# Performance work log

Hardware: AMD Instinct MI355X
Metric: run time of the kernel (lower is better)

Reference implementation:

```python
import jax, jax.numpy as jnp
import numpy as np

B, C, NS, NP = 8, 128, 32, 128  # batch, channels, nsample, npoint


def setup_inputs() -> dict:
    key = jax.random.key(0)
    k1, k2 = jax.random.split(key)
    points = jax.random.normal(k1, (B, C, NS, NP), dtype=jnp.float32)
    gamma = jax.random.uniform(k2, (1,), dtype=jnp.float32)
    return {"points": points, "gamma": gamma}


def reference(points, gamma):
    b, c, ns, npnt = points.shape
    x = points.reshape(b, c, ns * npnt)              # [B, C, N]
    # energy[b, n, m] = sum_c x[b,c,n] * x[b,c,m]   (QK^T with Q=K=x^T)
    energy = jnp.einsum('bcn,bcm->bnm', x, x)
    # max-subtraction variant: softmax(max_row - energy)
    energy_new = jnp.max(energy, axis=-1, keepdims=True) - energy
    attention = jax.nn.softmax(energy_new, axis=-1)   # [B, N, N]
    # points_attention = V @ attention^T : out[b,c,n] = sum_m x[b,c,m]*attn[b,n,m]
    out = jnp.einsum('bcm,bnm->bcn', x, attention)
    out = out.reshape(b, c, ns, npnt)
    return gamma * out + points
```

## Files before the change

kernel.cpp:

```cpp
#include <hip/hip_runtime.h>
#include <stdint.h>

#define NB_ 8
#define NC_ 128
#define NN_ 4096

typedef float f32x4 __attribute__((ext_vector_type(4)));
typedef _Float16 f16x8 __attribute__((ext_vector_type(8)));
typedef short s16x8 __attribute__((ext_vector_type(8)));
typedef unsigned short u16x4 __attribute__((ext_vector_type(4)));

__device__ __forceinline__ uint16_t f2bf(float f) {
    union { float f; uint32_t u; } v; v.f = f;
    return (uint16_t)((v.u + 0x7FFFu + ((v.u >> 16) & 1u)) >> 16);
}
__device__ __forceinline__ uint16_t f2bf_trunc(float f) {
    union { float f; uint32_t u; } v; v.f = f;
    return (uint16_t)(v.u >> 16);
}
__device__ __forceinline__ float bf2f(uint16_t b) {
    union { uint32_t u; float f; } v; v.u = ((uint32_t)b) << 16;
    return v.f;
}

__global__ __launch_bounds__(256) void prep_kernel(
        const float* __restrict__ pts, _Float16* __restrict__ xt,
        _Float16* __restrict__ Kf, uint16_t* __restrict__ Vf) {
    __shared__ float T[64][65];
    int bid = blockIdx.x;
    int ct = bid & 1, nt = (bid >> 1) & 63, b = bid >> 7;
    int c0 = ct * 64, n0 = nt * 64;
    int lr = threadIdx.x >> 6, lc = threadIdx.x & 63;
    const float* src = pts + ((size_t)b * NC_ + c0) * NN_ + n0;
#pragma unroll
    for (int r = 0; r < 16; ++r) {
        int cl = r * 4 + lr;
        T[cl][lc] = src[(size_t)cl * NN_ + lc];
    }
    __syncthreads();
#pragma unroll
    for (int r = 0; r < 16; ++r) {
        int nl = r * 4 + lr;
        xt[((size_t)b * NN_ + n0 + nl) * NC_ + c0 + lc] = (_Float16)T[lc][nl];
    }

    int w = threadIdx.x >> 6, l = threadIdx.x & 63, l15 = l & 15, g = l >> 4;
    _Float16* Kfb = Kf + (size_t)b * 524288;
    uint16_t* Vfb = Vf + (size_t)b * 524288;
#pragma unroll
    for (int e = 0; e < 2; ++e) {
        int q2 = w + e * 4;
        int tl = q2 >> 2, msq = (q2 >> 1) & 1, ccl = q2 & 1;
        int t = nt * 2 + tl, cc = ct * 2 + ccl;
        f16x8 kv;
#pragma unroll
        for (int j = 0; j < 8; ++j)
            kv[j] = (_Float16)T[ccl * 32 + g * 8 + j][tl * 32 + msq * 16 + l15];
        *(f16x8*)(Kfb + (((size_t)t * 8 + msq * 4 + cc) * 64 + l) * 8) = kv;
    }
#pragma unroll
    for (int e = 0; e < 2; ++e) {
        int q2 = w + e * 4;
        int tl = q2 >> 2, csl = q2 & 3;
        int t = nt * 2 + tl, cs = ct * 4 + csl;
        s16x8 vv;
#pragma unroll
        for (int j = 0; j < 8; ++j) {
            int m = (j < 4) ? (g * 4 + j) : (16 + g * 4 + (j - 4));
            vv[j] = (short)f2bf(T[csl * 16 + l15][tl * 32 + m]);
        }
        *(s16x8*)(Vfb + (((size_t)t * 8 + cs) * 64 + l) * 8) = vv;
    }
}

template <int MSPLIT>
__global__ __launch_bounds__(256, 3) void flash_kernel(
        const _Float16* __restrict__ xt, const _Float16* __restrict__ Kf,
        const uint16_t* __restrict__ Vf,
        uint16_t* __restrict__ Opart, float* __restrict__ lpart,
        const float* __restrict__ pts, const float* __restrict__ gamma,
        float* __restrict__ out) {
    int bid = blockIdx.x;
    int b = bid & 7;
    int rest = bid >> 3;
    int nb = rest & 31;
    int mh = rest >> 5;
    int tid = threadIdx.x;
    int w = tid >> 6, l = tid & 63, l15 = l & 15, g = l >> 4;

    __shared__ __align__(16) uint16_t Kt[2 * 4096];
    __shared__ __align__(16) uint16_t Vt[2 * 4096];

    int nbase = nb * 128 + w * 32;
    const _Float16* xtb = xt + (size_t)b * NN_ * NC_;
    const char* KfB = (const char*)(Kf + (size_t)b * 524288);
    const char* VfB = (const char*)(Vf + (size_t)b * 524288);
    char* KtB = (char*)Kt;
    char* VtB = (char*)Vt;
    int so = tid * 16;

#define STAGE(TILE, BUF) do {                                                          \
        size_t gb_ = (size_t)(TILE) * 8192 + so;                                       \
        int lb_ = (BUF) * 8192 + so;                                                   \
        __builtin_amdgcn_global_load_lds(                                              \
            (const __attribute__((address_space(1))) void*)(KfB + gb_),                \
            (__attribute__((address_space(3))) void*)(KtB + lb_), 16, 0, 0);           \
        __builtin_amdgcn_global_load_lds(                                              \
            (const __attribute__((address_space(1))) void*)(KfB + gb_ + 4096),         \
            (__attribute__((address_space(3))) void*)(KtB + lb_ + 4096), 16, 0, 0);    \
        __builtin_amdgcn_global_load_lds(                                              \
            (const __attribute__((address_space(1))) void*)(VfB + gb_),                \
            (__attribute__((address_space(3))) void*)(VtB + lb_), 16, 0, 0);           \
        __builtin_amdgcn_global_load_lds(                                              \
            (const __attribute__((address_space(1))) void*)(VfB + gb_ + 4096),         \
            (__attribute__((address_space(3))) void*)(VtB + lb_ + 4096), 16, 0, 0);    \
    } while (0)

    f16x8 q[2][4];
#pragma unroll
    for (int ns = 0; ns < 2; ++ns)
#pragma unroll
        for (int cc = 0; cc < 4; ++cc)
            q[ns][cc] = *(const f16x8*)(xtb + (size_t)(nbase + ns * 16 + l15) * NC_ + cc * 32 + g * 8);

    f32x4 acc[8][2];
#pragma unroll
    for (int cs = 0; cs < 8; ++cs)
#pragma unroll
        for (int ns = 0; ns < 2; ++ns)
            acc[cs][ns] = (f32x4){0.f, 0.f, 0.f, 0.f};
    float lsum[2] = {0.f, 0.f};

    const int nsteps = (MSPLIT == 3) ? (mh < 2 ? 43 : 42) : 128;
    const int tile0 = (MSPLIT == 3) ? (mh * 43) : 0;

    STAGE(tile0, 0);

    for (int it = 0; it < nsteps; ++it) {
        __syncthreads();
        int cur = it & 1, nxt = cur ^ 1;
        if (it + 1 < nsteps) STAGE(tile0 + it + 1, nxt);

        const _Float16* Kc = (const _Float16*)(Kt + cur * 4096);
        const uint16_t* Vc = Vt + cur * 4096;

        s16x8 pf[2];
#pragma unroll
        for (int ms = 0; ms < 2; ++ms) {
            f16x8 kf[4];
#pragma unroll
            for (int cc = 0; cc < 4; ++cc)
                kf[cc] = *(const f16x8*)(Kc + (ms * 4 + cc) * 512 + l * 8);

            f32x4 s[2];
            s[0] = (f32x4){0.f, 0.f, 0.f, 0.f};
            s[1] = (f32x4){0.f, 0.f, 0.f, 0.f};
            __builtin_amdgcn_s_setprio(1);
#pragma unroll
            for (int cc = 0; cc < 4; ++cc)
#pragma unroll
                for (int ns = 0; ns < 2; ++ns)
                    s[ns] = __builtin_amdgcn_mfma_f32_16x16x32_f16(kf[cc], q[ns][cc], s[ns], 0, 0, 0);
            __builtin_amdgcn_s_setprio(0);
#pragma unroll
            for (int ns = 0; ns < 2; ++ns) {
                float p0 = __expf(-(s[ns][0] + 64.f));
                float p1 = __expf(-(s[ns][1] + 64.f));
                float p2 = __expf(-(s[ns][2] + 64.f));
                float p3 = __expf(-(s[ns][3] + 64.f));
                lsum[ns] += (p0 + p1) + (p2 + p3);
                pf[ns][ms * 4 + 0] = (short)f2bf_trunc(p0);
                pf[ns][ms * 4 + 1] = (short)f2bf_trunc(p1);
                pf[ns][ms * 4 + 2] = (short)f2bf_trunc(p2);
                pf[ns][ms * 4 + 3] = (short)f2bf_trunc(p3);
            }
        }

        __builtin_amdgcn_s_setprio(1);
#pragma unroll
        for (int cs = 0; cs < 8; ++cs) {
            s16x8 vf = *(const s16x8*)(Vc + cs * 512 + l * 8);
#pragma unroll
            for (int ns = 0; ns < 2; ++ns)
                acc[cs][ns] = __builtin_amdgcn_mfma_f32_16x16x32_bf16(vf, pf[ns], acc[cs][ns], 0, 0, 0);
        }
        __builtin_amdgcn_s_setprio(0);
    }
#undef STAGE

    float lred[2], linv[2];
#pragma unroll
    for (int ns = 0; ns < 2; ++ns) {
        float v2 = lsum[ns];
        v2 += __shfl_xor(v2, 16);
        v2 += __shfl_xor(v2, 32);
        lred[ns] = v2;
        linv[ns] = 1.0f / v2;
    }

    if (MSPLIT > 1) {
        uint16_t* opb = Opart + (size_t)((b * 32 + nb) * MSPLIT + mh) * 16384;
#pragma unroll
        for (int cs = 0; cs < 8; ++cs)
#pragma unroll
            for (int ns = 0; ns < 2; ++ns)
#pragma unroll
                for (int r = 0; r < 4; ++r)
                    opb[(cs * 16 + g * 4 + r) * 128 + w * 32 + ns * 16 + l15] =
                        f2bf(acc[cs][ns][r] * linv[ns]);
        if (g == 0) {
            size_t lb = (size_t)((b * 32 + nb) * MSPLIT + mh) * 128;
#pragma unroll
            for (int ns = 0; ns < 2; ++ns)
                lpart[lb + w * 32 + ns * 16 + l15] = lred[ns];
        }
    } else {
        float gm = gamma[0];
        const float* ptsb = pts + (size_t)b * NC_ * NN_;
        float* outb = out + (size_t)b * NC_ * NN_;
#pragma unroll
        for (int cs = 0; cs < 8; ++cs)
#pragma unroll
            for (int ns = 0; ns < 2; ++ns)
#pragma unroll
                for (int r = 0; r < 4; ++r) {
                    size_t idx = (size_t)(cs * 16 + g * 4 + r) * NN_ + nbase + ns * 16 + l15;
                    outb[idx] = gm * acc[cs][ns][r] * linv[ns] + ptsb[idx];
                }
    }
}

template <int NS>
__global__ __launch_bounds__(256) void epi_kernel(
        const float* __restrict__ pts, const float* __restrict__ gamma,
        const uint16_t* __restrict__ Opart, const float* __restrict__ lpart,
        float* __restrict__ out) {
    size_t t = (size_t)blockIdx.x * 256 + threadIdx.x;
    size_t e = t * 4;
    int b = (int)(e >> 19);
    int r = (int)(e & 524287);
    int c = r >> 12;
    int n = r & 4095;
    int nb = n >> 7, nl = n & 127;
    int base = (b * 32 + nb) * NS;
    f32x4 osum = (f32x4){0.f, 0.f, 0.f, 0.f};
    f32x4 lsum = (f32x4){0.f, 0.f, 0.f, 0.f};
#pragma unroll
    for (int i = 0; i < NS; ++i) {
        u16x4 o16 = *(const u16x4*)(Opart + (size_t)(base + i) * 16384 + c * 128 + nl);
        f32x4 li = *(const f32x4*)(lpart + (size_t)(base + i) * 128 + nl);
#pragma unroll
        for (int j = 0; j < 4; ++j) {
            osum[j] += bf2f(o16[j]) * li[j];
            lsum[j] += li[j];
        }
    }
    f32x4 p = *(const f32x4*)(pts + e);
    float gm = gamma[0];
    f32x4 res;
#pragma unroll
    for (int j = 0; j < 4; ++j)
        res[j] = gm * osum[j] / lsum[j] + p[j];
    *(f32x4*)(out + e) = res;
}

extern "C" void kernel_launch(void* const* d_in, const int* in_sizes, int n_in,
                              void* d_out, int out_size, void* d_ws, size_t ws_size,
                              hipStream_t stream) {
    const float* pts = (const float*)d_in[0];
    const float* gamma = (const float*)d_in[1];
    float* out = (float*)d_out;

    char* ws = (char*)d_ws;
    _Float16* xt = (_Float16*)ws;
    _Float16* Kf = (_Float16*)(ws + 8388608);
    uint16_t* Vf = (uint16_t*)(ws + 16777216);
    uint16_t* Opart = (uint16_t*)(ws + 25165824);
    float* lpart = (float*)(ws + 25165824 + 25165824);
    const size_t WS3 = 25165824ull + 25165824ull + 393216ull;

    prep_kernel<<<1024, 256, 0, stream>>>(pts, xt, Kf, Vf);
    if (ws_size >= WS3) {
        flash_kernel<3><<<768, 256, 0, stream>>>(xt, Kf, Vf, Opart, lpart, pts, gamma, out);
        epi_kernel<3><<<4096, 256, 0, stream>>>(pts, gamma, Opart, lpart, out);
    } else {
        flash_kernel<1><<<256, 256, 0, stream>>>(xt, Kf, Vf, nullptr, nullptr, pts, gamma, out);
    }
}
```

Before: 93.20 us.

## Load K/V tiles directly into registers and switch to a 2-way key split

Removes the LDS double-buffered global_load_lds staging and the per-iteration __syncthreads. Each wave now reads K and V fragments straight from global memory into registers, with the next K tile prefetched into a register ping-pong buffer. The key-dimension split goes from 3 to 2 (512 blocks) and launch bounds drop to 2 blocks per CU to make room for the extra registers. The aim is to cut barrier and LDS overhead, but every wave now fetches K/V separately through L2 instead of sharing one LDS copy per block, and there are fewer blocks in flight.

```diff
diff --git a/kernel.cpp b/kernel.cpp
--- a/kernel.cpp
+++ b/kernel.cpp
@@ -74,7 +74,7 @@
 }
 
 template <int MSPLIT>
-__global__ __launch_bounds__(256, 3) void flash_kernel(
+__global__ __launch_bounds__(256, 2) void flash_kernel(
         const _Float16* __restrict__ xt, const _Float16* __restrict__ Kf,
         const uint16_t* __restrict__ Vf,
         uint16_t* __restrict__ Opart, float* __restrict__ lpart,
@@ -88,33 +88,10 @@
     int tid = threadIdx.x;
     int w = tid >> 6, l = tid & 63, l15 = l & 15, g = l >> 4;
 
-    __shared__ __align__(16) uint16_t Kt[2 * 4096];
-    __shared__ __align__(16) uint16_t Vt[2 * 4096];
-
     int nbase = nb * 128 + w * 32;
     const _Float16* xtb = xt + (size_t)b * NN_ * NC_;
-    const char* KfB = (const char*)(Kf + (size_t)b * 524288);
-    const char* VfB = (const char*)(Vf + (size_t)b * 524288);
-    char* KtB = (char*)Kt;
-    char* VtB = (char*)Vt;
-    int so = tid * 16;
-
-#define STAGE(TILE, BUF) do {                                                          \
-        size_t gb_ = (size_t)(TILE) * 8192 + so;                                       \
-        int lb_ = (BUF) * 8192 + so;                                                   \
-        __builtin_amdgcn_global_load_lds(                                              \
-            (const __attribute__((address_space(1))) void*)(KfB + gb_),                \
-            (__attribute__((address_space(3))) void*)(KtB + lb_), 16, 0, 0);           \
-        __builtin_amdgcn_global_load_lds(                                              \
-            (const __attribute__((address_space(1))) void*)(KfB + gb_ + 4096),         \
-            (__attribute__((address_space(3))) void*)(KtB + lb_ + 4096), 16, 0, 0);    \
-        __builtin_amdgcn_global_load_lds(                                              \
-            (const __attribute__((address_space(1))) void*)(VfB + gb_),                \
-            (__attribute__((address_space(3))) void*)(VtB + lb_), 16, 0, 0);           \
-        __builtin_amdgcn_global_load_lds(                                              \
-            (const __attribute__((address_space(1))) void*)(VfB + gb_ + 4096),         \
-            (__attribute__((address_space(3))) void*)(VtB + lb_ + 4096), 16, 0, 0);    \
-    } while (0)
+    const _Float16* Kfb = Kf + (size_t)b * 524288 + (size_t)l * 8;
+    const uint16_t* Vfb = Vf + (size_t)b * 524288 + (size_t)l * 8;
 
     f16x8 q[2][4];
 #pragma unroll
@@ -131,62 +108,71 @@
             acc[cs][ns] = (f32x4){0.f, 0.f, 0.f, 0.f};
     float lsum[2] = {0.f, 0.f};
 
-    const int nsteps = (MSPLIT == 3) ? (mh < 2 ? 43 : 42) : 128;
-    const int tile0 = (MSPLIT == 3) ? (mh * 43) : 0;
-
-    STAGE(tile0, 0);
-
-    for (int it = 0; it < nsteps; ++it) {
-        __syncthreads();
-        int cur = it & 1, nxt = cur ^ 1;
-        if (it + 1 < nsteps) STAGE(tile0 + it + 1, nxt);
-
-        const _Float16* Kc = (const _Float16*)(Kt + cur * 4096);
-        const uint16_t* Vc = Vt + cur * 4096;
-
-        s16x8 pf[2];
-#pragma unroll
-        for (int ms = 0; ms < 2; ++ms) {
-            f16x8 kf[4];
-#pragma unroll
-            for (int cc = 0; cc < 4; ++cc)
-                kf[cc] = *(const f16x8*)(Kc + (ms * 4 + cc) * 512 + l * 8);
-
-            f32x4 s[2];
-            s[0] = (f32x4){0.f, 0.f, 0.f, 0.f};
-            s[1] = (f32x4){0.f, 0.f, 0.f, 0.f};
-            __builtin_amdgcn_s_setprio(1);
-#pragma unroll
-            for (int cc = 0; cc < 4; ++cc)
-#pragma unroll
-                for (int ns = 0; ns < 2; ++ns)
-                    s[ns] = __builtin_amdgcn_mfma_f32_16x16x32_f16(kf[cc], q[ns][cc], s[ns], 0, 0, 0);
-            __builtin_amdgcn_s_setprio(0);
-#pragma unroll
-            for (int ns = 0; ns < 2; ++ns) {
-                float p0 = __expf(-(s[ns][0] + 64.f));
-                float p1 = __expf(-(s[ns][1] + 64.f));
-                float p2 = __expf(-(s[ns][2] + 64.f));
-                float p3 = __expf(-(s[ns][3] + 64.f));
-                lsum[ns] += (p0 + p1) + (p2 + p3);
-                pf[ns][ms * 4 + 0] = (short)f2bf_trunc(p0);
-                pf[ns][ms * 4 + 1] = (short)f2bf_trunc(p1);
-                pf[ns][ms * 4 + 2] = (short)f2bf_trunc(p2);
-                pf[ns][ms * 4 + 3] = (short)f2bf_trunc(p3);
-            }
-        }
-
-        __builtin_amdgcn_s_setprio(1);
-#pragma unroll
-        for (int cs = 0; cs < 8; ++cs) {
-            s16x8 vf = *(const s16x8*)(Vc + cs * 512 + l * 8);
-#pragma unroll
-            for (int ns = 0; ns < 2; ++ns)
-                acc[cs][ns] = __builtin_amdgcn_mfma_f32_16x16x32_bf16(vf, pf[ns], acc[cs][ns], 0, 0, 0);
-        }
-        __builtin_amdgcn_s_setprio(0);
-    }
-#undef STAGE
+    const int nsteps = (MSPLIT == 2) ? 64 : 128;
+    const int tile0 = mh * nsteps;
+
+    f16x8 ka[8], kb[8];
+#pragma unroll
+    for (int c8 = 0; c8 < 8; ++c8)
+        ka[c8] = *(const f16x8*)(Kfb + (size_t)tile0 * 4096 + c8 * 512);
+
+#define FLASH_STEP(IT, KC, KN) do {                                                     \
+        int t_ = tile0 + (IT);                                                          \
+              \
+        s16x8 vf[8];                                                                    \
+        _Pragma("unroll")                                                               \
+        for (int cs = 0; cs < 8; ++cs)                                                  \
+            vf[cs] = *(const s16x8*)(Vfb + (size_t)t_ * 4096 + cs * 512);               \
+                                                  \
+        if ((IT) + 1 < nsteps) {                                                        \
+            _Pragma("unroll")                                                           \
+            for (int c8 = 0; c8 < 8; ++c8)                                              \
+                KN[c8] = *(const f16x8*)(Kfb + (size_t)(t_ + 1) * 4096 + c8 * 512);     \
+        }                                                                               \
+        s16x8 pf[2];                                                                    \
+        _Pragma("unroll")                                                               \
+        for (int ms = 0; ms < 2; ++ms) {                                                \
+                           \
+            f32x4 s[2];                                                                 \
+            s[0] = (f32x4){0.f, 0.f, 0.f, 0.f};                                         \
+            s[1] = (f32x4){0.f, 0.f, 0.f, 0.f};                                         \
+            __builtin_amdgcn_s_setprio(1);                                              \
+            _Pragma("unroll")                                                           \
+            for (int cc = 0; cc < 4; ++cc)                                              \
+                _Pragma("unroll")                                                       \
+                for (int ns = 0; ns < 2; ++ns)                                          \
+                    s[ns] = __builtin_amdgcn_mfma_f32_16x16x32_f16(                     \
+                        KC[ms * 4 + cc], q[ns][cc], s[ns], 0, 0, 0);                    \
+            __builtin_amdgcn_s_setprio(0);                                              \
+            _Pragma("unroll")                                                           \
+            for (int ns = 0; ns < 2; ++ns) {                                            \
+                float p0 = __expf(-(s[ns][0] + 64.f));                                  \
+                float p1 = __expf(-(s[ns][1] + 64.f));                                  \
+                float p2 = __expf(-(s[ns][2] + 64.f));                                  \
+                float p3 = __expf(-(s[ns][3] + 64.f));                                  \
+                lsum[ns] += (p0 + p1) + (p2 + p3);                                      \
+                pf[ns][ms * 4 + 0] = (short)f2bf_trunc(p0);                             \
+                pf[ns][ms * 4 + 1] = (short)f2bf_trunc(p1);                             \
+                pf[ns][ms * 4 + 2] = (short)f2bf_trunc(p2);                             \
+                pf[ns][ms * 4 + 3] = (short)f2bf_trunc(p3);                             \
+            }                                                                           \
+        }                                                                               \
+                    \
+        __builtin_amdgcn_s_setprio(1);                                                  \
+        _Pragma("unroll")                                                               \
+        for (int cs = 0; cs < 8; ++cs)                                                  \
+            _Pragma("unroll")                                                           \
+            for (int ns = 0; ns < 2; ++ns)                                              \
+                acc[cs][ns] = __builtin_amdgcn_mfma_f32_16x16x32_bf16(                  \
+                    vf[cs], pf[ns], acc[cs][ns], 0, 0, 0);                              \
+        __builtin_amdgcn_s_setprio(0);                                                  \
+    } while (0)
+
+    for (int it = 0; it < nsteps; it += 2) {
+        FLASH_STEP(it, ka, kb);
+        FLASH_STEP(it + 1, kb, ka);
+    }
+#undef FLASH_STEP
 
     float lred[2], linv[2];
 #pragma unroll
@@ -276,13 +262,13 @@
     _Float16* Kf = (_Float16*)(ws + 8388608);
     uint16_t* Vf = (uint16_t*)(ws + 16777216);
     uint16_t* Opart = (uint16_t*)(ws + 25165824);
-    float* lpart = (float*)(ws + 25165824 + 25165824);
-    const size_t WS3 = 25165824ull + 25165824ull + 393216ull;
+    float* lpart = (float*)(ws + 25165824 + 16777216);
+    const size_t WS2 = 25165824ull + 16777216ull + 262144ull;
 
     prep_kernel<<<1024, 256, 0, stream>>>(pts, xt, Kf, Vf);
-    if (ws_size >= WS3) {
-        flash_kernel<3><<<768, 256, 0, stream>>>(xt, Kf, Vf, Opart, lpart, pts, gamma, out);
-        epi_kernel<3><<<4096, 256, 0, stream>>>(pts, gamma, Opart, lpart, out);
+    if (ws_size >= WS2) {
+        flash_kernel<2><<<512, 256, 0, stream>>>(xt, Kf, Vf, Opart, lpart, pts, gamma, out);
+        epi_kernel<2><<<4096, 256, 0, stream>>>(pts, gamma, Opart, lpart, out);
     } else {
         flash_kernel<1><<<256, 256, 0, stream>>>(xt, Kf, Vf, nullptr, nullptr, pts, gamma, out);
     }
```

Measured after the change: 100.8 us. +8.2%, slower.

## Triple-buffer K/V tiles in LDS with prefetch two steps ahead

Applied to the files above, without the earlier changes.

Replaces the double-buffered K/V shared-memory staging with a three-slot ring buffer, issuing global-to-LDS loads two iterations ahead. Explicit vmcnt waits let the current tile's loads complete while the next tile's loads stay in flight, with a raw s_barrier in place of __syncthreads. This is meant to hide global load latency behind the MFMA work. LDS use rises from 32KB to 48KB per block, which may lower occupancy below the 3 blocks per CU requested in launch bounds.

```diff
diff --git a/kernel.cpp b/kernel.cpp
--- a/kernel.cpp
+++ b/kernel.cpp
@@ -88,32 +88,30 @@
     int tid = threadIdx.x;
     int w = tid >> 6, l = tid & 63, l15 = l & 15, g = l >> 4;
 
-    __shared__ __align__(16) uint16_t Kt[2 * 4096];
-    __shared__ __align__(16) uint16_t Vt[2 * 4096];
+    __shared__ __align__(16) uint16_t KV[3 * 8192];
 
     int nbase = nb * 128 + w * 32;
     const _Float16* xtb = xt + (size_t)b * NN_ * NC_;
     const char* KfB = (const char*)(Kf + (size_t)b * 524288);
     const char* VfB = (const char*)(Vf + (size_t)b * 524288);
-    char* KtB = (char*)Kt;
-    char* VtB = (char*)Vt;
+    char* KVB = (char*)KV;
     int so = tid * 16;
 
-#define STAGE(TILE, BUF) do {                                                          \
+#define STAGE(TILE, BUFOFF) do {                                                       \
         size_t gb_ = (size_t)(TILE) * 8192 + so;                                       \
-        int lb_ = (BUF) * 8192 + so;                                                   \
+        int lb_ = (BUFOFF) + so;                                                       \
         __builtin_amdgcn_global_load_lds(                                              \
             (const __attribute__((address_space(1))) void*)(KfB + gb_),                \
-            (__attribute__((address_space(3))) void*)(KtB + lb_), 16, 0, 0);           \
+            (__attribute__((address_space(3))) void*)(KVB + lb_), 16, 0, 0);           \
         __builtin_amdgcn_global_load_lds(                                              \
             (const __attribute__((address_space(1))) void*)(KfB + gb_ + 4096),         \
-            (__attribute__((address_space(3))) void*)(KtB + lb_ + 4096), 16, 0, 0);    \
+            (__attribute__((address_space(3))) void*)(KVB + lb_ + 4096), 16, 0, 0);    \
         __builtin_amdgcn_global_load_lds(                                              \
             (const __attribute__((address_space(1))) void*)(VfB + gb_),                \
-            (__attribute__((address_space(3))) void*)(VtB + lb_), 16, 0, 0);           \
+            (__attribute__((address_space(3))) void*)(KVB + lb_ + 8192), 16, 0, 0);    \
         __builtin_amdgcn_global_load_lds(                                              \
             (const __attribute__((address_space(1))) void*)(VfB + gb_ + 4096),         \
-            (__attribute__((address_space(3))) void*)(VtB + lb_ + 4096), 16, 0, 0);    \
+            (__attribute__((address_space(3))) void*)(KVB + lb_ + 12288), 16, 0, 0);   \
     } while (0)
 
     f16x8 q[2][4];
@@ -134,15 +132,25 @@
     const int nsteps = (MSPLIT == 3) ? (mh < 2 ? 43 : 42) : 128;
     const int tile0 = (MSPLIT == 3) ? (mh * 43) : 0;
 
+    asm volatile("s_waitcnt vmcnt(0)" ::: "memory");
     STAGE(tile0, 0);
-
+    STAGE(tile0 + 1, 16384);
+
+    int cb = 0;
     for (int it = 0; it < nsteps; ++it) {
-        __syncthreads();
-        int cur = it & 1, nxt = cur ^ 1;
-        if (it + 1 < nsteps) STAGE(tile0 + it + 1, nxt);
-
-        const _Float16* Kc = (const _Float16*)(Kt + cur * 4096);
-        const uint16_t* Vc = Vt + cur * 4096;
+        if (it < nsteps - 1) {
+            asm volatile("s_waitcnt vmcnt(4)" ::: "memory");
+        } else {
+            asm volatile("s_waitcnt vmcnt(0)" ::: "memory");
+        }
+        __builtin_amdgcn_s_barrier();
+        if (it + 2 < nsteps) {
+            int b2 = cb + 2; if (b2 >= 3) b2 -= 3;
+            STAGE(tile0 + it + 2, b2 * 16384);
+        }
+
+        const _Float16* Kc = (const _Float16*)(KVB + cb * 16384);
+        const uint16_t* Vc = (const uint16_t*)(KVB + cb * 16384 + 8192);
 
         s16x8 pf[2];
 #pragma unroll
@@ -185,6 +193,8 @@
                 acc[cs][ns] = __builtin_amdgcn_mfma_f32_16x16x32_bf16(vf, pf[ns], acc[cs][ns], 0, 0, 0);
         }
         __builtin_amdgcn_s_setprio(0);
+
+        ++cb; if (cb >= 3) cb = 0;
     }
 #undef STAGE
 
```

New measurement: 92.04 us. No clear change (-1.2%).
